# Optimization experiments

Measured on AMD Instinct MI355X. Metric: run time of the kernel, lower is better.

## Reference

```python
import jax, jax.numpy as jnp
import numpy as np

B, S, D_IN, D_OUT, H = 2, 2048, 1024, 1024, 16
HD = D_OUT // H

def setup_inputs() -> dict:
    key = jax.random.key(0)
    ks = jax.random.split(key, 6)
    sc_in = 1.0 / np.sqrt(D_IN)
    sc_out = 1.0 / np.sqrt(D_OUT)
    return {
        "x": jax.random.normal(ks[0], (B, S, D_IN), dtype=jnp.float32),
        "Wq": jax.random.uniform(ks[1], (D_IN, D_OUT), jnp.float32, -sc_in, sc_in),
        "Wk": jax.random.uniform(ks[2], (D_IN, D_OUT), jnp.float32, -sc_in, sc_in),
        "Wv": jax.random.uniform(ks[3], (D_IN, D_OUT), jnp.float32, -sc_in, sc_in),
        "Wo": jax.random.uniform(ks[4], (D_OUT, D_OUT), jnp.float32, -sc_out, sc_out),
        "bo": jax.random.uniform(ks[5], (D_OUT,), jnp.float32, -sc_out, sc_out),
    }

def reference(x, Wq, Wk, Wv, Wo, bo):
    b, s, _ = x.shape
    # QKV projections (no bias), split heads -> [b, h, s, hd]
    q = (x @ Wq).reshape(b, s, H, HD).transpose(0, 2, 1, 3)
    k = (x @ Wk).reshape(b, s, H, HD).transpose(0, 2, 1, 3)
    v = (x @ Wv).reshape(b, s, H, HD).transpose(0, 2, 1, 3)
    scores = jnp.einsum('bhqd,bhkd->bhqk', q, k)
    causal = jnp.triu(jnp.ones((s, s), dtype=bool), k=1)
    scores = jnp.where(causal, -jnp.inf, scores)
    w = jax.nn.softmax(scores / np.sqrt(HD), axis=-1)  # dropout p=0.0 -> identity
    ctx = jnp.einsum('bhqk,bhkd->bhqd', w, v)
    ctx = ctx.transpose(0, 2, 1, 3).reshape(b, s, D_OUT)
    return ctx @ Wo + bo
```

## Files before the change

kernel.cpp:

```cpp
#include <hip/hip_runtime.h>
#include <stdint.h>

typedef unsigned short u16;
typedef __attribute__((ext_vector_type(8))) short short8;
typedef __attribute__((ext_vector_type(4))) float floatx4;
typedef __attribute__((ext_vector_type(4))) u16 ushort4v;

typedef __attribute__((address_space(1))) const uint32_t gu32;
typedef __attribute__((address_space(3))) uint32_t lu32;

#define MFMA(a, b, c) __builtin_amdgcn_mfma_f32_16x16x32_bf16((a), (b), (c), 0, 0, 0)

#define QSCALE 0.1803368801111204f

__device__ __forceinline__ u16 f2bf(float f) {
    union { float f; uint32_t u; } x; x.f = f;
    uint32_t u = x.u;
    u += 0x7fffu + ((u >> 16) & 1u);
    return (u16)(u >> 16);
}

__device__ __forceinline__ uint32_t pack_trunc(float hi, float lo) {
    return __builtin_amdgcn_perm(__float_as_uint(hi), __float_as_uint(lo), 0x07060302u);
}

__device__ __forceinline__ void async16(u16* lds, const u16* g) {
    __builtin_amdgcn_global_load_lds((gu32*)g, (lu32*)lds, 16, 0, 0);
}


__global__ __launch_bounds__(256) void prep_kernel(
    const float* __restrict__ x,
    const float* __restrict__ W0, const float* __restrict__ W1,
    const float* __restrict__ W2, const float* __restrict__ W3,
    u16* __restrict__ WT, u16* __restrict__ Xbf)
{
    const int z = blockIdx.z;
    const int tx = threadIdx.x, ty = threadIdx.y;
    if (z == 4) {
        const int bid = blockIdx.y * 32 + blockIdx.x;
        const int t = ty * 32 + tx;
        const size_t base = ((size_t)bid * 256 + t) * 16;
        const int row = (int)(base >> 10);
        const int col0 = (int)(base & 1023);
        const int key = (row >> 1) & 3;
        const int grp = col0 & ~31;
        const int c0 = (col0 >> 3) & 3;
        const float* xf = x + base;
        short8 v0, v1;
#pragma unroll
        for (int j = 0; j < 8; j++) v0[j] = (short)f2bf(xf[j]);
#pragma unroll
        for (int j = 0; j < 8; j++) v1[j] = (short)f2bf(xf[8 + j]);
        u16* dr = Xbf + (size_t)row * 1024 + grp;
        *(short8*)&dr[(c0 ^ key) << 3] = v0;
        *(short8*)&dr[((c0 + 1) ^ key) << 3] = v1;
        return;
    }
    __shared__ u16 tile[32][33];
    const float* W = (z == 0) ? W0 : (z == 1) ? W1 : (z == 2) ? W2 : W3;
    u16* dst = WT + (size_t)z * 1024 * 1024;
    const int n0 = blockIdx.x * 32, k0 = blockIdx.y * 32;
#pragma unroll
    for (int i = 0; i < 4; i++)
        tile[ty + i * 8][tx] = f2bf(W[(size_t)(k0 + ty + i * 8) * 1024 + n0 + tx]);
    __syncthreads();
#pragma unroll
    for (int i = 0; i < 4; i++) {
        const int n = n0 + ty + i * 8;
        const int key = (n >> 1) & 3;
        const int sc = k0 + (((((tx >> 3) & 3) ^ key)) << 3) + (tx & 7);
        dst[(size_t)n * 1024 + sc] = tile[tx][ty + i * 8];
    }
}

__global__ __launch_bounds__(256) void gemm_qkv_kernel(
    const u16* __restrict__ X, const u16* __restrict__ WT,
    u16* __restrict__ Q, u16* __restrict__ Kout, u16* __restrict__ VT)
{
    __shared__ __align__(16) u16 As[128 * 32];
    __shared__ __align__(16) u16 Bs[128 * 32];
    const int bid = blockIdx.x;
    const int xcd = bid & 7;
    const int idx = bid >> 3;
    const int mat = idx >> 5;
    const int rr  = (idx >> 3) & 3;
    const int nn  = idx & 7;
    const int m0 = (xcd * 4 + rr) * 128;
    const int n0 = nn * 128;
    const u16* BW = WT + (size_t)mat * 1024 * 1024;
    const int tid = threadIdx.x;
    const int wave = tid >> 6, lane = tid & 63;
    const int lrow = lane & 15, lquad = lane >> 4;
    const int wr = (wave >> 1) * 64, wc = (wave & 1) * 64;
    const int fragoff = ((lquad ^ ((lrow >> 1) & 3)) << 3);

    const int ci0 = wave * 128 + lane;
    const int ci1 = ci0 + 64;
    const int ar0 = ci0 >> 2, ac0 = (ci0 & 3) * 8;
    const int ar1 = ci1 >> 2, ac1 = (ci1 & 3) * 8;
    u16* ldsA0 = As + (size_t)(wave * 128) * 8;
    u16* ldsA1 = As + (size_t)(wave * 128 + 64) * 8;
    u16* ldsB0 = Bs + (size_t)(wave * 128) * 8;
    u16* ldsB1 = Bs + (size_t)(wave * 128 + 64) * 8;
    const u16* gA0 = &X[(size_t)(m0 + ar0) * 1024 + ac0];
    const u16* gA1 = &X[(size_t)(m0 + ar1) * 1024 + ac1];
    const u16* gB0 = &BW[(size_t)(n0 + ar0) * 1024 + ac0];
    const u16* gB1 = &BW[(size_t)(n0 + ar1) * 1024 + ac1];

    floatx4 acc[4][4];
#pragma unroll
    for (int mt = 0; mt < 4; mt++)
#pragma unroll
        for (int nt = 0; nt < 4; nt++) acc[mt][nt] = (floatx4){0.f, 0.f, 0.f, 0.f};

    for (int k0 = 0; k0 < 1024; k0 += 32) {
        __syncthreads();
        async16(ldsA0, gA0 + k0);
        async16(ldsA1, gA1 + k0);
        async16(ldsB0, gB0 + k0);
        async16(ldsB1, gB1 + k0);
        __syncthreads();
        short8 af[4], bf[4];
#pragma unroll
        for (int mt = 0; mt < 4; mt++)
            af[mt] = *(const short8*)&As[(wr + mt * 16 + lrow) * 32 + fragoff];
#pragma unroll
        for (int nt = 0; nt < 4; nt++)
            bf[nt] = *(const short8*)&Bs[(wc + nt * 16 + lrow) * 32 + fragoff];
#pragma unroll
        for (int mt = 0; mt < 4; mt++)
#pragma unroll
            for (int nt = 0; nt < 4; nt++)
                acc[mt][nt] = MFMA(af[mt], bf[nt], acc[mt][nt]);
    }

#pragma unroll
    for (int mt = 0; mt < 4; mt++) {
        const int gm = m0 + wr + mt * 16 + lquad * 4;
        const int b_ = gm >> 11;
        const int s  = gm & 2047;
        const int kt = s >> 6;
        const int r  = s & 63;
#pragma unroll
        for (int nt = 0; nt < 4; nt++) {
            const int gn = n0 + wc + nt * 16 + lrow;
            const int h = gn >> 6, hd = gn & 63;
            const int bh = b_ * 16 + h;
            if (mat == 2) {
                const size_t base = ((size_t)(bh * 32 + kt) * 64 + hd) * 64
                                  + ((((r >> 3) ^ (hd & 7)) << 3) | (r & 7));
                ushort4v v;
#pragma unroll
                for (int i = 0; i < 4; i++) v[i] = f2bf(acc[mt][nt][i]);
                *(ushort4v*)&VT[base] = v;
            } else if (mat == 1) {
#pragma unroll
                for (int i = 0; i < 4; i++) {
                    const int r2 = r + i;
                    Kout[((size_t)(bh * 32 + kt) * 64 + r2) * 64
                         + (((hd >> 3) ^ (r2 & 7)) << 3) + (hd & 7)] = f2bf(acc[mt][nt][i]);
                }
            } else {
#pragma unroll
                for (int i = 0; i < 4; i++)
                    Q[((size_t)bh * 2048 + s + i) * 64 + hd] = f2bf(acc[mt][nt][i] * QSCALE);
            }
        }
    }
}

__global__ __launch_bounds__(256, 4) void attn_kernel(
    const u16* __restrict__ Q, const u16* __restrict__ Ksw,
    const u16* __restrict__ Vsw, u16* __restrict__ ctx)
{
    __shared__ __align__(16) u16 Ks[2][4096];
    __shared__ __align__(16) u16 Vs[2][4096];
    __shared__ __align__(16) u16 P[4][1024];
    const int tid = threadIdx.x, wave = tid >> 6, lane = tid & 63;
    const int lrow = lane & 15, lquad = lane >> 4;
    const float NEGINF = -__builtin_inff();

    const int bh = blockIdx.x & 31;
    const int g = blockIdx.x >> 5;
    const int qb = (g < 16) ? (31 - g) : (g - 16);
    const int ntiles = qb + 1;
    const int q0 = qb * 64 + wave * 16;

    const u16* Qb = Q   + (size_t)bh * 2048 * 64;
    const u16* Kt = Ksw + (size_t)bh * 32 * 4096;
    const u16* Vt = Vsw + (size_t)bh * 32 * 4096;

    const short8 qf0 = *(const short8*)&Qb[(size_t)(q0 + lrow) * 64 + lquad * 8];
    const short8 qf1 = *(const short8*)&Qb[(size_t)(q0 + lrow) * 64 + 32 + lquad * 8];

    const int r7 = lrow & 7;
    int koff0[4], koff1[4], voff[2][4];
#pragma unroll
    for (int nt = 0; nt < 4; nt++) {
        const int row = nt * 16 + lrow;
        koff0[nt] = row * 64 + ((lquad ^ r7) << 3);
        koff1[nt] = row * 64 + (((4 + lquad) ^ r7) << 3);
    }
#pragma unroll
    for (int st = 0; st < 2; st++)
#pragma unroll
        for (int ht = 0; ht < 4; ht++) {
            const int row = ht * 16 + lrow;
            voff[st][ht] = row * 64 + (((st * 4 + lquad) ^ r7) << 3);
        }
    int pwoff[4], proff[2];
#pragma unroll
    for (int nt = 0; nt < 4; nt++)
        pwoff[nt] = lrow * 64 + (((nt * 2 + (lquad >> 1)) ^ r7) << 3) + ((lquad & 1) << 2);
#pragma unroll
    for (int st = 0; st < 2; st++)
        proff[st] = lrow * 64 + (((st * 4 + lquad) ^ r7) << 3);

    const int myq = q0 + lrow;
    float m_s = NEGINF, l_s = 0.f;
    floatx4 o[4];
#pragma unroll
    for (int i = 0; i < 4; i++) o[i] = (floatx4){0.f, 0.f, 0.f, 0.f};

    const int co0 = wave * 1024;
    const int co1 = wave * 1024 + 512;
    const int lo8 = lane * 8;

    async16(&Ks[0][co0], Kt + co0 + lo8);
    async16(&Ks[0][co1], Kt + co1 + lo8);
    async16(&Vs[0][co0], Vt + co0 + lo8);
    async16(&Vs[0][co1], Vt + co1 + lo8);

    u16* Pw = P[wave];

    for (int kt = 0; kt < ntiles; kt++) {
        __syncthreads();
        if (kt + 1 < ntiles) {
            const u16* Kn = Kt + (size_t)(kt + 1) * 4096;
            const u16* Vn = Vt + (size_t)(kt + 1) * 4096;
            const int nb = (kt + 1) & 1;
            async16(&Ks[nb][co0], Kn + co0 + lo8);
            async16(&Ks[nb][co1], Kn + co1 + lo8);
            async16(&Vs[nb][co0], Vn + co0 + lo8);
            async16(&Vs[nb][co1], Vn + co1 + lo8);
        }
        const u16* kbuf = Ks[kt & 1];
        const u16* vbuf = Vs[kt & 1];

        floatx4 s[4];
#pragma unroll
        for (int nt = 0; nt < 4; nt++) {
            const short8 kf0 = *(const short8*)&kbuf[koff0[nt]];
            const short8 kf1 = *(const short8*)&kbuf[koff1[nt]];
            floatx4 a = (floatx4){0.f, 0.f, 0.f, 0.f};
            a = MFMA(kf0, qf0, a);
            a = MFMA(kf1, qf1, a);
            s[nt] = a;
        }

        const bool diag = (kt == ntiles - 1);
        if (diag) {
#pragma unroll
            for (int nt = 0; nt < 4; nt++)
#pragma unroll
                for (int i = 0; i < 4; i++)
                    if (kt * 64 + nt * 16 + lquad * 4 + i > myq) s[nt][i] = NEGINF;
        }
        float mx = NEGINF;
#pragma unroll
        for (int nt = 0; nt < 4; nt++)
#pragma unroll
            for (int i = 0; i < 4; i++) mx = fmaxf(mx, s[nt][i]);
        mx = fmaxf(mx, __shfl_xor(mx, 16));
        mx = fmaxf(mx, __shfl_xor(mx, 32));
        const float mnew = fmaxf(m_s, mx);
        const float alpha = exp2f(m_s - mnew);
        m_s = mnew;
        float sum = 0.f;
#pragma unroll
        for (int nt = 0; nt < 4; nt++)
#pragma unroll
            for (int i = 0; i < 4; i++) {
                const float pv = exp2f(s[nt][i] - mnew);
                s[nt][i] = pv;
                sum += pv;
            }
        sum += __shfl_xor(sum, 16);
        sum += __shfl_xor(sum, 32);
        l_s = l_s * alpha + sum;
#pragma unroll
        for (int ht = 0; ht < 4; ht++)
#pragma unroll
            for (int i = 0; i < 4; i++) o[ht][i] *= alpha;

#pragma unroll
        for (int nt = 0; nt < 4; nt++) {
            uint2 pk;
            pk.x = pack_trunc(s[nt][1], s[nt][0]);
            pk.y = pack_trunc(s[nt][3], s[nt][2]);
            *(uint2*)&Pw[pwoff[nt]] = pk;
        }
#pragma unroll
        for (int st = 0; st < 2; st++) {
            const short8 pf = *(const short8*)&Pw[proff[st]];
#pragma unroll
            for (int ht = 0; ht < 4; ht++) {
                const short8 vf = *(const short8*)&vbuf[voff[st][ht]];
                o[ht] = MFMA(vf, pf, o[ht]);
            }
        }
    }

    const int b_ = bh >> 4, h_ = bh & 15;
    const float inv_l = 1.0f / l_s;
    const int skey = (lrow >> 1) & 3;
#pragma unroll
    for (int ht = 0; ht < 4; ht++) {
        uint32_t pk0 = (uint32_t)f2bf(o[ht][0] * inv_l) | ((uint32_t)f2bf(o[ht][1] * inv_l) << 16);
        uint32_t pk1 = (uint32_t)f2bf(o[ht][2] * inv_l) | ((uint32_t)f2bf(o[ht][3] * inv_l) << 16);
        uint2 pk = {pk0, pk1};
        const int col = h_ * 64 + ((ht >> 1) << 5)
                      + (((((ht & 1) << 1) | (lquad >> 1)) ^ skey) << 3)
                      + ((lquad & 1) << 2);
        *(uint2*)&ctx[((size_t)(b_ * 2048 + q0 + lrow)) * 1024 + col] = pk;
    }
}

__global__ __launch_bounds__(256) void gemm_out_kernel(
    const u16* __restrict__ X, const u16* __restrict__ WT,
    const float* __restrict__ bias, float* __restrict__ out)
{
    __shared__ __align__(16) u16 As[128 * 32];
    __shared__ __align__(16) u16 Bs[128 * 32];
    const int bid = blockIdx.x;
    const int xcd = bid & 7;
    const int idx = bid >> 3;
    const int rr  = idx >> 3;
    const int nn  = idx & 7;
    const int m0 = (xcd * 4 + rr) * 128;
    const int n0 = nn * 128;
    const int tid = threadIdx.x;
    const int wave = tid >> 6, lane = tid & 63;
    const int lrow = lane & 15, lquad = lane >> 4;
    const int wr = (wave >> 1) * 64, wc = (wave & 1) * 64;
    const int fragoff = ((lquad ^ ((lrow >> 1) & 3)) << 3);

    const int ci0 = wave * 128 + lane;
    const int ci1 = ci0 + 64;
    const int ar0 = ci0 >> 2, ac0 = (ci0 & 3) * 8;
    const int ar1 = ci1 >> 2, ac1 = (ci1 & 3) * 8;
    u16* ldsA0 = As + (size_t)(wave * 128) * 8;
    u16* ldsA1 = As + (size_t)(wave * 128 + 64) * 8;
    u16* ldsB0 = Bs + (size_t)(wave * 128) * 8;
    u16* ldsB1 = Bs + (size_t)(wave * 128 + 64) * 8;
    const u16* gA0 = &X[(size_t)(m0 + ar0) * 1024 + ac0];
    const u16* gA1 = &X[(size_t)(m0 + ar1) * 1024 + ac1];
    const u16* gB0 = &WT[(size_t)(n0 + ar0) * 1024 + ac0];
    const u16* gB1 = &WT[(size_t)(n0 + ar1) * 1024 + ac1];

    floatx4 acc[4][4];
#pragma unroll
    for (int mt = 0; mt < 4; mt++)
#pragma unroll
        for (int nt = 0; nt < 4; nt++) acc[mt][nt] = (floatx4){0.f, 0.f, 0.f, 0.f};

    for (int k0 = 0; k0 < 1024; k0 += 32) {
        __syncthreads();
        async16(ldsA0, gA0 + k0);
        async16(ldsA1, gA1 + k0);
        async16(ldsB0, gB0 + k0);
        async16(ldsB1, gB1 + k0);
        __syncthreads();
        short8 af[4], bf[4];
#pragma unroll
        for (int mt = 0; mt < 4; mt++)
            af[mt] = *(const short8*)&As[(wr + mt * 16 + lrow) * 32 + fragoff];
#pragma unroll
        for (int nt = 0; nt < 4; nt++)
            bf[nt] = *(const short8*)&Bs[(wc + nt * 16 + lrow) * 32 + fragoff];
#pragma unroll
        for (int mt = 0; mt < 4; mt++)
#pragma unroll
            for (int nt = 0; nt < 4; nt++)
                acc[mt][nt] = MFMA(af[mt], bf[nt], acc[mt][nt]);
    }

#pragma unroll
    for (int mt = 0; mt < 4; mt++) {
        const int gm = m0 + wr + mt * 16 + lquad * 4;
#pragma unroll
        for (int nt = 0; nt < 4; nt++) {
            const int gn = n0 + wc + nt * 16 + lrow;
            const float bv = bias[gn];
#pragma unroll
            for (int i = 0; i < 4; i++)
                out[(size_t)(gm + i) * 1024 + gn] = acc[mt][nt][i] + bv;
        }
    }
}

extern "C" void kernel_launch(void* const* d_in, const int* in_sizes, int n_in,
                              void* d_out, int out_size, void* d_ws, size_t ws_size,
                              hipStream_t stream) {
    u16* ws = (u16*)d_ws + 64;

    const size_t MB1 = 1024 * 1024;
    u16* WT   = ws;
    u16* Qw   = ws + 4 * MB1;
    u16* Kw   = ws + 8 * MB1;
    u16* VTw  = ws + 12 * MB1;
    u16* ctxw = ws + 16 * MB1;
    u16* Xbf  = ws + 20 * MB1;

    prep_kernel<<<dim3(32, 32, 5), dim3(32, 8), 0, stream>>>(
        (const float*)d_in[0], (const float*)d_in[1], (const float*)d_in[2],
        (const float*)d_in[3], (const float*)d_in[4], WT, Xbf);
    gemm_qkv_kernel<<<768, 256, 0, stream>>>(Xbf, WT, Qw, Kw, VTw);
    attn_kernel<<<1024, 256, 0, stream>>>(Qw, Kw, VTw, ctxw);
    gemm_out_kernel<<<256, 256, 0, stream>>>(ctxw, WT + 3 * MB1, (const float*)d_in[5], (float*)d_out);
}
```

Before: 195.4 us.

## Process two 64-row query blocks per attention workgroup to reuse K/V tiles

Each attention workgroup now handles 128 query rows, with every wave owning two 16-row query slices, A and B. Each K/V tile loaded into shared memory and each K fragment read from LDS is shared by both slices, which halves the grid and the K/V global traffic per query. Slice A skips the final tile, where it is fully masked. In exchange the kernel uses more registers (launch bounds drop to 2 blocks per CU), has fewer workgroups to balance the causal load, and makes each wave do more serial work.

```diff
diff --git a/kernel.cpp b/kernel.cpp
--- a/kernel.cpp
+++ b/kernel.cpp
@@ -170,29 +170,32 @@
     }
 }
 
-__global__ __launch_bounds__(256, 4) void attn_kernel(
+__global__ __launch_bounds__(256, 2) void attn_kernel(
     const u16* __restrict__ Q, const u16* __restrict__ Ksw,
     const u16* __restrict__ Vsw, u16* __restrict__ ctx)
 {
     __shared__ __align__(16) u16 Ks[2][4096];
     __shared__ __align__(16) u16 Vs[2][4096];
-    __shared__ __align__(16) u16 P[4][1024];
+    __shared__ __align__(16) u16 P[8192];
     const int tid = threadIdx.x, wave = tid >> 6, lane = tid & 63;
     const int lrow = lane & 15, lquad = lane >> 4;
     const float NEGINF = -__builtin_inff();
 
     const int bh = blockIdx.x & 31;
     const int g = blockIdx.x >> 5;
-    const int qb = (g < 16) ? (31 - g) : (g - 16);
-    const int ntiles = qb + 1;
-    const int q0 = qb * 64 + wave * 16;
-
-    const u16* Qb = Q   + (size_t)bh * 2048 * 64;
+    const int Qb = (g < 8) ? (15 - g) : (g - 8);
+    const int ntiles = 2 * Qb + 2;
+    const int qA = Qb * 128 + wave * 16;
+    const int qB = qA + 64;
+
+    const u16* Qp = Q   + (size_t)bh * 2048 * 64;
     const u16* Kt = Ksw + (size_t)bh * 32 * 4096;
     const u16* Vt = Vsw + (size_t)bh * 32 * 4096;
 
-    const short8 qf0 = *(const short8*)&Qb[(size_t)(q0 + lrow) * 64 + lquad * 8];
-    const short8 qf1 = *(const short8*)&Qb[(size_t)(q0 + lrow) * 64 + 32 + lquad * 8];
+    const short8 qfA0 = *(const short8*)&Qp[(size_t)(qA + lrow) * 64 + lquad * 8];
+    const short8 qfA1 = *(const short8*)&Qp[(size_t)(qA + lrow) * 64 + 32 + lquad * 8];
+    const short8 qfB0 = *(const short8*)&Qp[(size_t)(qB + lrow) * 64 + lquad * 8];
+    const short8 qfB1 = *(const short8*)&Qp[(size_t)(qB + lrow) * 64 + 32 + lquad * 8];
 
     const int r7 = lrow & 7;
     int koff0[4], koff1[4], voff[2][4];
@@ -217,11 +220,14 @@
     for (int st = 0; st < 2; st++)
         proff[st] = lrow * 64 + (((st * 4 + lquad) ^ r7) << 3);
 
-    const int myq = q0 + lrow;
-    float m_s = NEGINF, l_s = 0.f;
-    floatx4 o[4];
-#pragma unroll
-    for (int i = 0; i < 4; i++) o[i] = (floatx4){0.f, 0.f, 0.f, 0.f};
+    const int myqA = qA + lrow, myqB = qB + lrow;
+    float mA = NEGINF, lA = 0.f, mB = NEGINF, lB = 0.f;
+    floatx4 oA[4], oB[4];
+#pragma unroll
+    for (int i = 0; i < 4; i++) {
+        oA[i] = (floatx4){0.f, 0.f, 0.f, 0.f};
+        oB[i] = (floatx4){0.f, 0.f, 0.f, 0.f};
+    }
 
     const int co0 = wave * 1024;
     const int co1 = wave * 1024 + 512;
@@ -232,7 +238,8 @@
     async16(&Vs[0][co0], Vt + co0 + lo8);
     async16(&Vs[0][co1], Vt + co1 + lo8);
 
-    u16* Pw = P[wave];
+    u16* PA = P + wave * 2048;
+    u16* PB = PA + 1024;
 
     for (int kt = 0; kt < ntiles; kt++) {
         __syncthreads();
@@ -248,82 +255,152 @@
         const u16* kbuf = Ks[kt & 1];
         const u16* vbuf = Vs[kt & 1];
 
-        floatx4 s[4];
+        const bool doA = (kt < ntiles - 1);
+        const bool diagA = (kt == ntiles - 2);
+        const bool diagB = (kt == ntiles - 1);
+
+        short8 kf0[4], kf1[4];
 #pragma unroll
         for (int nt = 0; nt < 4; nt++) {
-            const short8 kf0 = *(const short8*)&kbuf[koff0[nt]];
-            const short8 kf1 = *(const short8*)&kbuf[koff1[nt]];
-            floatx4 a = (floatx4){0.f, 0.f, 0.f, 0.f};
-            a = MFMA(kf0, qf0, a);
-            a = MFMA(kf1, qf1, a);
-            s[nt] = a;
-        }
-
-        const bool diag = (kt == ntiles - 1);
-        if (diag) {
+            kf0[nt] = *(const short8*)&kbuf[koff0[nt]];
+            kf1[nt] = *(const short8*)&kbuf[koff1[nt]];
+        }
+        floatx4 sA[4], sB[4];
+#pragma unroll
+        for (int nt = 0; nt < 4; nt++) {
+            floatx4 b = (floatx4){0.f, 0.f, 0.f, 0.f};
+            b = MFMA(kf0[nt], qfB0, b);
+            b = MFMA(kf1[nt], qfB1, b);
+            sB[nt] = b;
+        }
+        if (doA) {
+#pragma unroll
+            for (int nt = 0; nt < 4; nt++) {
+                floatx4 a = (floatx4){0.f, 0.f, 0.f, 0.f};
+                a = MFMA(kf0[nt], qfA0, a);
+                a = MFMA(kf1[nt], qfA1, a);
+                sA[nt] = a;
+            }
+        }
+
+        if (diagB) {
 #pragma unroll
             for (int nt = 0; nt < 4; nt++)
 #pragma unroll
                 for (int i = 0; i < 4; i++)
-                    if (kt * 64 + nt * 16 + lquad * 4 + i > myq) s[nt][i] = NEGINF;
-        }
-        float mx = NEGINF;
+                    if (kt * 64 + nt * 16 + lquad * 4 + i > myqB) sB[nt][i] = NEGINF;
+        }
+        float mxB = NEGINF;
 #pragma unroll
         for (int nt = 0; nt < 4; nt++)
 #pragma unroll
-            for (int i = 0; i < 4; i++) mx = fmaxf(mx, s[nt][i]);
-        mx = fmaxf(mx, __shfl_xor(mx, 16));
-        mx = fmaxf(mx, __shfl_xor(mx, 32));
-        const float mnew = fmaxf(m_s, mx);
-        const float alpha = exp2f(m_s - mnew);
-        m_s = mnew;
-        float sum = 0.f;
+            for (int i = 0; i < 4; i++) mxB = fmaxf(mxB, sB[nt][i]);
+        mxB = fmaxf(mxB, __shfl_xor(mxB, 16));
+        mxB = fmaxf(mxB, __shfl_xor(mxB, 32));
+        const float mnB = fmaxf(mB, mxB);
+        const float alB = exp2f(mB - mnB);
+        mB = mnB;
+        float smB = 0.f;
 #pragma unroll
         for (int nt = 0; nt < 4; nt++)
 #pragma unroll
             for (int i = 0; i < 4; i++) {
-                const float pv = exp2f(s[nt][i] - mnew);
-                s[nt][i] = pv;
-                sum += pv;
-            }
-        sum += __shfl_xor(sum, 16);
-        sum += __shfl_xor(sum, 32);
-        l_s = l_s * alpha + sum;
+                const float pv = exp2f(sB[nt][i] - mnB);
+                sB[nt][i] = pv;
+                smB += pv;
+            }
+        smB += __shfl_xor(smB, 16);
+        smB += __shfl_xor(smB, 32);
+        lB = lB * alB + smB;
 #pragma unroll
         for (int ht = 0; ht < 4; ht++)
 #pragma unroll
-            for (int i = 0; i < 4; i++) o[ht][i] *= alpha;
-
+            for (int i = 0; i < 4; i++) oB[ht][i] *= alB;
 #pragma unroll
         for (int nt = 0; nt < 4; nt++) {
             uint2 pk;
-            pk.x = pack_trunc(s[nt][1], s[nt][0]);
-            pk.y = pack_trunc(s[nt][3], s[nt][2]);
-            *(uint2*)&Pw[pwoff[nt]] = pk;
-        }
+            pk.x = pack_trunc(sB[nt][1], sB[nt][0]);
+            pk.y = pack_trunc(sB[nt][3], sB[nt][2]);
+            *(uint2*)&PB[pwoff[nt]] = pk;
+        }
+
+        if (doA) {
+            if (diagA) {
+#pragma unroll
+                for (int nt = 0; nt < 4; nt++)
+#pragma unroll
+                    for (int i = 0; i < 4; i++)
+                        if (kt * 64 + nt * 16 + lquad * 4 + i > myqA) sA[nt][i] = NEGINF;
+            }
+            float mxA = NEGINF;
+#pragma unroll
+            for (int nt = 0; nt < 4; nt++)
+#pragma unroll
+                for (int i = 0; i < 4; i++) mxA = fmaxf(mxA, sA[nt][i]);
+            mxA = fmaxf(mxA, __shfl_xor(mxA, 16));
+            mxA = fmaxf(mxA, __shfl_xor(mxA, 32));
+            const float mnA = fmaxf(mA, mxA);
+            const float alA = exp2f(mA - mnA);
+            mA = mnA;
+            float smA = 0.f;
+#pragma unroll
+            for (int nt = 0; nt < 4; nt++)
+#pragma unroll
+                for (int i = 0; i < 4; i++) {
+                    const float pv = exp2f(sA[nt][i] - mnA);
+                    sA[nt][i] = pv;
+                    smA += pv;
+                }
+            smA += __shfl_xor(smA, 16);
+            smA += __shfl_xor(smA, 32);
+            lA = lA * alA + smA;
+#pragma unroll
+            for (int ht = 0; ht < 4; ht++)
+#pragma unroll
+                for (int i = 0; i < 4; i++) oA[ht][i] *= alA;
+#pragma unroll
+            for (int nt = 0; nt < 4; nt++) {
+                uint2 pk;
+                pk.x = pack_trunc(sA[nt][1], sA[nt][0]);
+                pk.y = pack_trunc(sA[nt][3], sA[nt][2]);
+                *(uint2*)&PA[pwoff[nt]] = pk;
+            }
+        }
+
 #pragma unroll
         for (int st = 0; st < 2; st++) {
-            const short8 pf = *(const short8*)&Pw[proff[st]];
+            const short8 pfB = *(const short8*)&PB[proff[st]];
 #pragma unroll
             for (int ht = 0; ht < 4; ht++) {
                 const short8 vf = *(const short8*)&vbuf[voff[st][ht]];
-                o[ht] = MFMA(vf, pf, o[ht]);
+                oB[ht] = MFMA(vf, pfB, oB[ht]);
+            }
+            if (doA) {
+                const short8 pfA = *(const short8*)&PA[proff[st]];
+#pragma unroll
+                for (int ht = 0; ht < 4; ht++) {
+                    const short8 vf = *(const short8*)&vbuf[voff[st][ht]];
+                    oA[ht] = MFMA(vf, pfA, oA[ht]);
+                }
             }
         }
     }
 
     const int b_ = bh >> 4, h_ = bh & 15;
-    const float inv_l = 1.0f / l_s;
     const int skey = (lrow >> 1) & 3;
+    const float ivA = 1.0f / lA, ivB = 1.0f / lB;
 #pragma unroll
     for (int ht = 0; ht < 4; ht++) {
-        uint32_t pk0 = (uint32_t)f2bf(o[ht][0] * inv_l) | ((uint32_t)f2bf(o[ht][1] * inv_l) << 16);
-        uint32_t pk1 = (uint32_t)f2bf(o[ht][2] * inv_l) | ((uint32_t)f2bf(o[ht][3] * inv_l) << 16);
-        uint2 pk = {pk0, pk1};
         const int col = h_ * 64 + ((ht >> 1) << 5)
                       + (((((ht & 1) << 1) | (lquad >> 1)) ^ skey) << 3)
                       + ((lquad & 1) << 2);
-        *(uint2*)&ctx[((size_t)(b_ * 2048 + q0 + lrow)) * 1024 + col] = pk;
+        uint2 pkA, pkB;
+        pkA.x = (uint32_t)f2bf(oA[ht][0] * ivA) | ((uint32_t)f2bf(oA[ht][1] * ivA) << 16);
+        pkA.y = (uint32_t)f2bf(oA[ht][2] * ivA) | ((uint32_t)f2bf(oA[ht][3] * ivA) << 16);
+        pkB.x = (uint32_t)f2bf(oB[ht][0] * ivB) | ((uint32_t)f2bf(oB[ht][1] * ivB) << 16);
+        pkB.y = (uint32_t)f2bf(oB[ht][2] * ivB) | ((uint32_t)f2bf(oB[ht][3] * ivB) << 16);
+        *(uint2*)&ctx[((size_t)(b_ * 2048 + qA + lrow)) * 1024 + col] = pkA;
+        *(uint2*)&ctx[((size_t)(b_ * 2048 + qB + lrow)) * 1024 + col] = pkB;
     }
 }
 
@@ -417,6 +494,6 @@
         (const float*)d_in[0], (const float*)d_in[1], (const float*)d_in[2],
         (const float*)d_in[3], (const float*)d_in[4], WT, Xbf);
     gemm_qkv_kernel<<<768, 256, 0, stream>>>(Xbf, WT, Qw, Kw, VTw);
-    attn_kernel<<<1024, 256, 0, stream>>>(Qw, Kw, VTw, ctxw);
+    attn_kernel<<<512, 256, 0, stream>>>(Qw, Kw, VTw, ctxw);
     gemm_out_kernel<<<256, 256, 0, stream>>>(ctxw, WT + 3 * MB1, (const float*)d_in[5], (float*)d_out);
 }
```

Measured after the change: 211.2 us. 8.0% more time.
